# Kernel tuning notes

Hardware: AMD Instinct MI355X
Metric: run time of the kernel (lower is better)

## Reference

```python
import jax, jax.numpy as jnp
import numpy as np
import math

B = 262144
STATE = 6
TOTAL_MEAS = 27
HID = 256
INPUT_DIM = TOTAL_MEAS * 2 + 1 + STATE + 12  # 73
PI = math.pi
NORM_R_SCALE = 500.0 / 150000.0
ANG_IDX = np.array([0, 1, 3, 4, 6, 9, 10, 12, 13, 15, 18, 19, 21, 22, 24])
ANG_MASK = np.zeros((TOTAL_MEAS,), dtype=bool)
ANG_MASK[ANG_IDX] = True


def setup_inputs() -> dict:
    key = jax.random.key(0)
    ks = jax.random.split(key, 16)
    s = lambda fan: 1.0 / math.sqrt(fan)
    inp = {
        "meas": jax.random.normal(ks[0], (B, TOTAL_MEAS), jnp.float32),
        "mask": jnp.ones((B, TOTAL_MEAS), jnp.float32),
        "dt": jax.random.uniform(ks[1], (B,), jnp.float32),
        "baselines": jax.random.normal(ks[2], (B, 12), jnp.float32),
        "x_prev": jax.random.normal(ks[3], (B, STATE), jnp.float32),
        "hx": jnp.zeros((B, HID), jnp.float32),
        # GRU params (torch gate order: r, z, n)
        "W_ih": jax.random.uniform(ks[4], (3 * HID, INPUT_DIM), jnp.float32, -s(HID), s(HID)),
        "W_hh": jax.random.uniform(ks[5], (3 * HID, HID), jnp.float32, -s(HID), s(HID)),
        "b_ih": jax.random.uniform(ks[6], (3 * HID,), jnp.float32, -s(HID), s(HID)),
        "b_hh": jax.random.uniform(ks[7], (3 * HID,), jnp.float32, -s(HID), s(HID)),
        # LayerNorm
        "ln_g": jnp.ones((HID,), jnp.float32),
        "ln_b": jnp.zeros((HID,), jnp.float32),
        # MLP head: 256 -> 256 -> 128 -> 6*27
        "W1": jax.random.uniform(ks[8], (256, HID), jnp.float32, -s(HID), s(HID)),
        "b1": jax.random.uniform(ks[9], (256,), jnp.float32, -s(HID), s(HID)),
        "W2": jax.random.uniform(ks[10], (128, 256), jnp.float32, -s(256), s(256)),
        "b2": jax.random.uniform(ks[11], (128,), jnp.float32, -s(256), s(256)),
        "W3": jax.random.uniform(ks[12], (STATE * TOTAL_MEAS, 128), jnp.float32, -s(128), s(128)),
        "b3": jax.random.uniform(ks[13], (STATE * TOTAL_MEAS,), jnp.float32, -s(128), s(128)),
    }
    return inp


def _wrap_angle(a):
    two_pi = 2.0 * PI
    return a - two_pi * jnp.round(a / two_pi)


def _platform_y_pred(x_rel):
    # x_rel: [B, 6] -> [B, 9] radar/EO measurement
    r_xy = jnp.sqrt(x_rel[:, 0] ** 2 + x_rel[:, 2] ** 2 + 1e-9)
    az = jnp.arctan2(x_rel[:, 2], x_rel[:, 0]) / PI
    el = jnp.arctan2(x_rel[:, 4], r_xy) / PI
    r = jnp.sqrt(x_rel[:, 0] ** 2 + x_rel[:, 2] ** 2 + x_rel[:, 4] ** 2 + 1e-9)
    z = jnp.zeros_like(r)
    return jnp.stack([az, el, r, az, el, z, az, z, z], axis=1)


def _forward(meas, mask, dt, baselines, x_prev, hx,
             W_ih, W_hh, b_ih, b_hh, ln_g, ln_b, W1, b1, W2, b2, W3, b3):
    # f_predict (CV model): x0 += dt*x1, x2 += dt*x3, x4 += dt*x5
    dt_scaled = dt * NORM_R_SCALE  # [B]
    zcol = jnp.zeros_like(x_prev[:, :1])
    shift = jnp.concatenate([x_prev[:, 1:2], zcol, x_prev[:, 3:4], zcol, x_prev[:, 5:6], zcol], axis=1)
    x_minus = x_prev + dt_scaled[:, None] * shift  # [B, 6]

    y_pred = jnp.concatenate([
        _platform_y_pred(x_minus),
        _platform_y_pred(x_minus - baselines[:, 0:6]),
        _platform_y_pred(x_minus - baselines[:, 6:12]),
    ], axis=1)  # [B, 27]

    innov = meas - y_pred
    wrapped = _wrap_angle(innov * PI) / PI
    innov = jnp.where(jnp.asarray(ANG_MASK)[None, :], wrapped, innov)
    innov = innov * mask

    rnn_in = jnp.concatenate([innov, mask, dt[:, None], x_minus, baselines], axis=1)  # [B, 73]

    # single-step GRU (torch semantics, gate order r,z,n)
    gi = rnn_in @ W_ih.T + b_ih  # [B, 3H]
    gh = hx @ W_hh.T + b_hh      # [B, 3H]
    gi_r, gi_z, gi_n = jnp.split(gi, 3, axis=1)
    gh_r, gh_z, gh_n = jnp.split(gh, 3, axis=1)
    r = jax.nn.sigmoid(gi_r + gh_r)
    z = jax.nn.sigmoid(gi_z + gh_z)
    n = jnp.tanh(gi_n + r * gh_n)
    h_new = (1.0 - z) * n + z * hx  # [B, H]

    # LayerNorm
    mu = jnp.mean(h_new, axis=-1, keepdims=True)
    var = jnp.var(h_new, axis=-1, keepdims=True)
    h_ln = (h_new - mu) / jnp.sqrt(var + 1e-5) * ln_g + ln_b

    # MLP gain head (dropout inactive at inference)
    f1 = jax.nn.relu(h_ln @ W1.T + b1)
    f2 = jax.nn.relu(f1 @ W2.T + b2)
    K = (f2 @ W3.T + b3).reshape(-1, STATE, TOTAL_MEAS)
    K = jnp.clip(K, -3.0, 3.0)

    correction = jnp.einsum('bsm,bm->bs', K, innov)
    x_new = jnp.clip(x_minus + correction, -5.0, 5.0)
    return x_new, h_new


def reference(meas, mask, dt, baselines, x_prev, hx,
              W_ih, W_hh, b_ih, b_hh, ln_g, ln_b, W1, b1, W2, b2, W3, b3):
    return _forward(meas, mask, dt, baselines, x_prev, hx,
                    W_ih, W_hh, b_ih, b_hh, ln_g, ln_b, W1, b1, W2, b2, W3, b3)
```

## Files before the change

### kernel.cpp

```cpp
#include <hip/hip_runtime.h>
#include <math.h>

#define B_TOTAL  262144
#define ROWS     64
#define NWG      (B_TOTAL/ROWS)
#define NTHR     512
#define PI_F     3.14159265358979323846f
#define NORM_R   (500.0f/150000.0f)

typedef float  f32x4  __attribute__((ext_vector_type(4)));
typedef short  bf16x8 __attribute__((ext_vector_type(8)));

#define GRU_SLAB 24576
#define OFF_GRU  0
#define OFF_W1   (11*GRU_SLAB)
#define OFF_W2   (OFF_W1 + 8*8192)
#define OFF_W3   (OFF_W2 + 8*4096)
#define W_TOTAL  (OFF_W3 + 4*8192)

#define LDS_RBF2  0
#define LDS_HB    17408
#define LDS_STG   (LDS_HB + 32768)
#define LDS_XMC   (LDS_STG + 2*49152)
#define LDS_LNS   (LDS_XMC + 1536)
#define LDS_TOTAL (LDS_LNS + 2048)

#define WAIT_VM0 asm volatile("s_waitcnt vmcnt(0)" ::: "memory")
#define BARv     __builtin_amdgcn_s_barrier()

__device__ __forceinline__ ushort f2bf(float f){
    union { float f; unsigned u; } v; v.f = f;
    unsigned r = v.u + 0x7FFFu + ((v.u >> 16) & 1u);
    return (ushort)(r >> 16);
}
__device__ __forceinline__ float b2f(ushort u){
    union { unsigned u; float f; } v; v.u = ((unsigned)u) << 16;
    return v.f;
}
__device__ __forceinline__ float sigm(float x){ return 1.0f/(1.0f+__expf(-x)); }
__device__ __forceinline__ float tanh_(float x){ return 1.0f - 2.0f/(__expf(2.0f*x)+1.0f); }
__device__ __forceinline__ int swzb(int row, int k){
    return ((row<<9) + (k<<1)) ^ ((row&7)<<4);
}
__device__ __forceinline__ bf16x8 rdW(const char* gb, int col, int lk){
    int slot = lk ^ ((col >> 1) & 3);
    return *(const bf16x8*)(gb + col*64 + slot*16);
}
template<int N>
__device__ __forceinline__ void stage_lin(const ushort* src, char* dst, int w, int lane){
    #pragma unroll
    for (int i = 0; i < N; ++i) {
        __builtin_amdgcn_global_load_lds(
            (const __attribute__((address_space(1))) void*)(src + (size_t)(i*512 + w*64 + lane)*8),
            (__attribute__((address_space(3))) void*)(dst + i*8192 + w*1024),
            16, 0, 0);
    }
}
__device__ __forceinline__ void mm4(const char* gb, int colbase, int lr, int lk,
                                    bf16x8 a0, bf16x8 a1, f32x4 acc[2][4]){
    #pragma unroll
    for (int j = 0; j < 4; ++j) {
        bf16x8 wf = rdW(gb, colbase + j*16 + lr, lk);
        acc[0][j] = __builtin_amdgcn_mfma_f32_16x16x32_bf16(wf, a0, acc[0][j], 0,0,0);
        acc[1][j] = __builtin_amdgcn_mfma_f32_16x16x32_bf16(wf, a1, acc[1][j], 0,0,0);
    }
}

__global__ void prep_weights(const float* __restrict__ W_ih, const float* __restrict__ W_hh,
                             const float* __restrict__ W1, const float* __restrict__ W2,
                             const float* __restrict__ W3, ushort* __restrict__ ws)
{
    int id = blockIdx.x*256 + threadIdx.x;
    if (id >= W_TOTAL) return;
    float v = 0.0f;
    if (id < OFF_W1) {
        int slab = id / GRU_SLAB, u = id % GRU_SLAB;
        int gate = u >> 13, u2 = u & 8191;
        int col = u2 >> 5, v5 = u2 & 31, slot = v5 >> 3, e = v5 & 7;
        int kq = slot ^ ((col >> 1) & 3);
        int k = slab*32 + kq*8 + e;
        int rowz = gate*256 + col;
        v = (k < 73) ? W_ih[rowz*73 + k] : ((k < 96) ? 0.0f : W_hh[rowz*256 + (k-96)]);
    } else if (id < OFF_W2) {
        int t = id - OFF_W1, kb = t >> 13, u2 = t & 8191;
        int col = u2 >> 5, v5 = u2 & 31, slot = v5 >> 3, e = v5 & 7;
        int kq = slot ^ ((col >> 1) & 3);
        v = W1[col*256 + kb*32 + kq*8 + e];
    } else if (id < OFF_W3) {
        int t = id - OFF_W2, kb = t >> 12, u2 = t & 4095;
        int col = u2 >> 5, v5 = u2 & 31, slot = v5 >> 3, e = v5 & 7;
        int kq = slot ^ ((col >> 1) & 3);
        v = W2[col*256 + kb*32 + kq*8 + e];
    } else {
        int t = id - OFF_W3, kb = t >> 13, u2 = t & 8191;
        int col = u2 >> 5, v5 = u2 & 31, slot = v5 >> 3, e = v5 & 7;
        int kq = slot ^ ((col >> 1) & 3);
        int k = kb*32 + kq*8 + e;
        v = (col < 162) ? W3[col*128 + k] : 0.0f;
    }
    ws[id] = f2bf(v);
}

__global__ __launch_bounds__(NTHR, 1) void knet_mfma(
    const float* __restrict__ meas, const float* __restrict__ mask,
    const float* __restrict__ dt,   const float* __restrict__ baselines,
    const float* __restrict__ x_prev, const float* __restrict__ hx,
    const float* __restrict__ b_ih, const float* __restrict__ b_hh,
    const float* __restrict__ ln_g, const float* __restrict__ ln_b,
    const float* __restrict__ b1,   const float* __restrict__ b2,
    const float* __restrict__ b3,
    const ushort* __restrict__ ws,
    float* __restrict__ out)
{
    extern __shared__ char smem[];
    ushort* Rbu  = (ushort*)(smem + LDS_RBF2);
    char*   Hb   = smem + LDS_HB;
    char*   STG  = smem + LDS_STG;
    float*  xmc  = (float*)(smem + LDS_XMC);
    float*  lnscr= (float*)(smem + LDS_LNS);

    const int tid  = threadIdx.x;
    const int w    = __builtin_amdgcn_readfirstlane(tid >> 6);
    const int nq   = w & 3;
    const int mh   = w >> 2;
    const int lane = tid & 63;
    const int lr   = lane & 15;
    const int lk   = lane >> 4;
    const int lk8  = lk * 8;
    const int row0 = blockIdx.x * ROWS;
    const int mrow = mh*32 + lr;
    float* hout = out + (size_t)B_TOTAL*6;

    stage_lin<6>(ws + OFF_GRU, STG, w, lane);

    float* scr = (float*)(STG + 49152);
    {
        const size_t m0 = (size_t)row0*27;
        for (int i = tid; i < 1728; i += NTHR) scr[i]        = meas[m0 + i];
        for (int i = tid; i < 1728; i += NTHR) scr[1728 + i] = mask[m0 + i];
        const size_t b0 = (size_t)row0*12;
        for (int i = tid; i < 768; i += NTHR)  scr[3456 + i] = baselines[b0 + i];
        if (tid < 384) scr[4224 + tid] = x_prev[(size_t)row0*6 + tid];
        if (tid < 64)  scr[4608 + tid] = dt[row0 + tid];
        const size_t hbase = (size_t)row0 * 256;
        #pragma unroll
        for (int ii = 0; ii < 4; ++ii) {
            int cid = tid + ii*NTHR;
            int r  = cid >> 5;
            int k0 = (cid & 31) << 3;
            const float4* p = (const float4*)(hx + hbase + (size_t)r*256 + k0);
            float4 u = p[0], v2 = p[1];
            bf16x8 o;
            o[0]=(short)f2bf(u.x);  o[1]=(short)f2bf(u.y);  o[2]=(short)f2bf(u.z);  o[3]=(short)f2bf(u.w);
            o[4]=(short)f2bf(v2.x); o[5]=(short)f2bf(v2.y); o[6]=(short)f2bf(v2.z); o[7]=(short)f2bf(v2.w);
            *(bf16x8*)(Hb + swzb(r, k0)) = o;
        }
    }
    __syncthreads();

    if (w < 4) {
        const int row = lane;
        const float dtv = scr[4608 + row];
        const float dts = dtv * NORM_R;
        float xp[6], xm[6];
        #pragma unroll
        for (int s = 0; s < 6; ++s) xp[s] = scr[4224 + row*6 + s];
        xm[0] = xp[0] + dts*xp[1]; xm[1] = xp[1];
        xm[2] = xp[2] + dts*xp[3]; xm[3] = xp[3];
        xm[4] = xp[4] + dts*xp[5]; xm[5] = xp[5];
        if (w < 3) {
            float xr[6];
            #pragma unroll
            for (int s = 0; s < 6; ++s) {
                float b = (w == 0) ? 0.0f : scr[3456 + row*12 + (w-1)*6 + s];
                xr[s] = xm[s] - b;
            }
            float rxy = sqrtf(xr[0]*xr[0] + xr[2]*xr[2] + 1e-9f);
            float azv = atan2f(xr[2], xr[0]) * (1.0f/PI_F);
            float elv = atan2f(xr[4], rxy)   * (1.0f/PI_F);
            float rrv = sqrtf(xr[0]*xr[0] + xr[2]*xr[2] + xr[4]*xr[4] + 1e-9f);
            float y[9] = {azv, elv, rrv, azv, elv, 0.0f, azv, 0.0f, 0.0f};
            const bool ang[9] = {true,true,false,true,true,false,true,false,false};
            #pragma unroll
            for (int i = 0; i < 9; ++i) {
                int m = w*9 + i;
                float ms = scr[1728 + row*27 + m];
                float v  = scr[row*27 + m] - y[i];
                if (ang[i]) v = v - 2.0f*rintf(v*0.5f);
                v *= ms;
                Rbu[row*104 + m]      = f2bf(v);
                Rbu[row*104 + 27 + m] = f2bf(ms);
            }
        } else {
            Rbu[row*104 + 54] = f2bf(dtv);
            #pragma unroll
            for (int s = 0; s < 6; ++s) Rbu[row*104 + 55 + s] = f2bf(xm[s]);
            #pragma unroll
            for (int q = 0; q < 12; ++q) Rbu[row*104 + 61 + q] = f2bf(scr[3456 + row*12 + q]);
            #pragma unroll
            for (int k = 73; k < 96; ++k) Rbu[row*104 + k] = 0;
            #pragma unroll
            for (int s = 0; s < 6; ++s) xmc[row*6 + s] = xm[s];
        }
    }
    __syncthreads();

    f32x4 ar[2][4], az[2][4], agi[2][4], agh[2][4];
    #pragma unroll
    for (int i = 0; i < 2; ++i)
        #pragma unroll
        for (int j = 0; j < 4; ++j) {
            ar[i][j]=(f32x4){0,0,0,0}; az[i][j]=(f32x4){0,0,0,0};
            agi[i][j]=(f32x4){0,0,0,0}; agh[i][j]=(f32x4){0,0,0,0};
        }
    #pragma unroll
    for (int kb = 0; kb < 11; ++kb) {
        WAIT_VM0; BARv;
        if (kb < 10) stage_lin<6>(ws + OFF_GRU + (kb+1)*GRU_SLAB, STG + ((kb+1)&1)*49152, w, lane);
        else         stage_lin<6>(ws + OFF_W1,                    STG + 49152,            w, lane);
        const char* sb = STG + (kb&1)*49152;
        bf16x8 a0, a1;
        if (kb < 3) { a0 = *(const bf16x8*)(Rbu + mrow*104 + kb*32 + lk8);
                      a1 = *(const bf16x8*)(Rbu + (mrow+16)*104 + kb*32 + lk8); }
        else        { a0 = *(const bf16x8*)(Hb + swzb(mrow,    (kb-3)*32 + lk8));
                      a1 = *(const bf16x8*)(Hb + swzb(mrow+16, (kb-3)*32 + lk8)); }
        __builtin_amdgcn_s_setprio(1);
        mm4(sb,         nq*64, lr, lk, a0, a1, ar);
        mm4(sb + 16384, nq*64, lr, lk, a0, a1, az);
        if (kb < 3) mm4(sb + 32768, nq*64, lr, lk, a0, a1, agi);
        else        mm4(sb + 32768, nq*64, lr, lk, a0, a1, agh);
        __builtin_amdgcn_s_setprio(0);
    }

    f32x4 hnv[2][4];
    float lsum[2] = {0,0}, lsq[2] = {0,0};
    #pragma unroll
    for (int j = 0; j < 4; ++j) {
        const int c0 = nq*64 + j*16 + lk*4;
        f32x4 bir = *(const f32x4*)(b_ih + c0),        bhr = *(const f32x4*)(b_hh + c0);
        f32x4 biz = *(const f32x4*)(b_ih + 256 + c0),  bhz = *(const f32x4*)(b_hh + 256 + c0);
        f32x4 bin_= *(const f32x4*)(b_ih + 512 + c0),  bhn = *(const f32x4*)(b_hh + 512 + c0);
        #pragma unroll
        for (int i = 0; i < 2; ++i) {
            const int row = mh*32 + i*16 + lr;
            uint2 hxd = *(const uint2*)(Hb + swzb(row, c0));
            float hx_[4] = { b2f((ushort)(hxd.x & 0xffffu)), b2f((ushort)(hxd.x >> 16)),
                             b2f((ushort)(hxd.y & 0xffffu)), b2f((ushort)(hxd.y >> 16)) };
            f32x4 hn4;
            #pragma unroll
            for (int e = 0; e < 4; ++e) {
                float rg = sigm(ar[i][j][e] + bir[e] + bhr[e]);
                float zg = sigm(az[i][j][e] + biz[e] + bhz[e]);
                float ng = tanh_(agi[i][j][e] + bin_[e] + rg*(agh[i][j][e] + bhn[e]));
                float hn = (1.0f - zg)*ng + zg*hx_[e];
                hn4[e] = hn;
                lsum[i] += hn; lsq[i] += hn*hn;
            }
            hnv[i][j] = hn4;
            float4 st = { hn4[0], hn4[1], hn4[2], hn4[3] };
            *(float4*)(hout + (size_t)(row0+row)*256 + c0) = st;
        }
    }
    #pragma unroll
    for (int i = 0; i < 2; ++i) {
        lsum[i] += __shfl_xor(lsum[i], 16); lsum[i] += __shfl_xor(lsum[i], 32);
        lsq[i]  += __shfl_xor(lsq[i], 16);  lsq[i]  += __shfl_xor(lsq[i], 32);
    }
    if (lk == 0) {
        #pragma unroll
        for (int i = 0; i < 2; ++i) {
            const int row = mh*32 + i*16 + lr;
            lnscr[row*8 + nq*2 + 0] = lsum[i];
            lnscr[row*8 + nq*2 + 1] = lsq[i];
        }
    }
    __syncthreads();

    {
        float mu[2], rstd[2];
        #pragma unroll
        for (int i = 0; i < 2; ++i) {
            const int row = mh*32 + i*16 + lr;
            float s = 0, q = 0;
            #pragma unroll
            for (int qq = 0; qq < 4; ++qq) { s += lnscr[row*8 + qq*2]; q += lnscr[row*8 + qq*2 + 1]; }
            mu[i] = s * (1.0f/256.0f);
            rstd[i] = rsqrtf(q*(1.0f/256.0f) - mu[i]*mu[i] + 1e-5f);
        }
        #pragma unroll
        for (int j = 0; j < 4; ++j) {
            const int c0 = nq*64 + j*16 + lk*4;
            f32x4 g4 = *(const f32x4*)(ln_g + c0);
            f32x4 b4 = *(const f32x4*)(ln_b + c0);
            #pragma unroll
            for (int i = 0; i < 2; ++i) {
                const int row = mh*32 + i*16 + lr;
                float v0 = (hnv[i][j][0]-mu[i])*rstd[i]*g4[0] + b4[0];
                float v1 = (hnv[i][j][1]-mu[i])*rstd[i]*g4[1] + b4[1];
                float v2 = (hnv[i][j][2]-mu[i])*rstd[i]*g4[2] + b4[2];
                float v3 = (hnv[i][j][3]-mu[i])*rstd[i]*g4[3] + b4[3];
                uint2 o;
                o.x = (unsigned)f2bf(v0) | ((unsigned)f2bf(v1) << 16);
                o.y = (unsigned)f2bf(v2) | ((unsigned)f2bf(v3) << 16);
                *(uint2*)(Hb + swzb(row, c0)) = o;
            }
        }
    }
    __syncthreads();

    f32x4 c2[2][4];
    #pragma unroll
    for (int i = 0; i < 2; ++i)
        #pragma unroll
        for (int j = 0; j < 4; ++j) c2[i][j] = (f32x4){0,0,0,0};
    WAIT_VM0; BARv;
    stage_lin<6>(ws + OFF_W1 + 3*8192, STG, w, lane);
    {
        const char* sb = STG + 49152;
        #pragma unroll
        for (int kb = 0; kb < 3; ++kb) {
            bf16x8 a0 = *(const bf16x8*)(Hb + swzb(mrow,    kb*32 + lk8));
            bf16x8 a1 = *(const bf16x8*)(Hb + swzb(mrow+16, kb*32 + lk8));
            __builtin_amdgcn_s_setprio(1);
            mm4(sb + kb*16384, nq*64, lr, lk, a0, a1, c2);
            __builtin_amdgcn_s_setprio(0);
        }
    }
    WAIT_VM0; BARv;
    stage_lin<4>(ws + OFF_W1 + 6*8192, STG + 49152, w, lane);
    {
        const char* sb = STG;
        #pragma unroll
        for (int kb = 3; kb < 6; ++kb) {
            bf16x8 a0 = *(const bf16x8*)(Hb + swzb(mrow,    kb*32 + lk8));
            bf16x8 a1 = *(const bf16x8*)(Hb + swzb(mrow+16, kb*32 + lk8));
            __builtin_amdgcn_s_setprio(1);
            mm4(sb + (kb-3)*16384, nq*64, lr, lk, a0, a1, c2);
            __builtin_amdgcn_s_setprio(0);
        }
    }
    WAIT_VM0; BARv;
    stage_lin<4>(ws + OFF_W2, STG, w, lane);
    {
        const char* sb = STG + 49152;
        #pragma unroll
        for (int kb = 6; kb < 8; ++kb) {
            bf16x8 a0 = *(const bf16x8*)(Hb + swzb(mrow,    kb*32 + lk8));
            bf16x8 a1 = *(const bf16x8*)(Hb + swzb(mrow+16, kb*32 + lk8));
            __builtin_amdgcn_s_setprio(1);
            mm4(sb + (kb-6)*16384, nq*64, lr, lk, a0, a1, c2);
            __builtin_amdgcn_s_setprio(0);
        }
    }
    __syncthreads();
    #pragma unroll
    for (int j = 0; j < 4; ++j) {
        const int c0 = nq*64 + j*16 + lk*4;
        f32x4 b4 = *(const f32x4*)(b1 + c0);
        #pragma unroll
        for (int i = 0; i < 2; ++i) {
            const int row = mh*32 + i*16 + lr;
            uint2 o;
            o.x = (unsigned)f2bf(fmaxf(c2[i][j][0]+b4[0],0.f)) | ((unsigned)f2bf(fmaxf(c2[i][j][1]+b4[1],0.f)) << 16);
            o.y = (unsigned)f2bf(fmaxf(c2[i][j][2]+b4[2],0.f)) | ((unsigned)f2bf(fmaxf(c2[i][j][3]+b4[3],0.f)) << 16);
            *(uint2*)(Hb + swzb(row, c0)) = o;
        }
    }
    __syncthreads();

    f32x4 c3[2][2];
    #pragma unroll
    for (int i = 0; i < 2; ++i)
        #pragma unroll
        for (int j = 0; j < 2; ++j) c3[i][j] = (f32x4){0,0,0,0};
    WAIT_VM0; BARv;
    stage_lin<4>(ws + OFF_W2 + 4*4096, STG + 49152, w, lane);
    {
        const char* sb = STG;
        #pragma unroll
        for (int kb = 0; kb < 4; ++kb) {
            bf16x8 a0 = *(const bf16x8*)(Hb + swzb(mrow,    kb*32 + lk8));
            bf16x8 a1 = *(const bf16x8*)(Hb + swzb(mrow+16, kb*32 + lk8));
            __builtin_amdgcn_s_setprio(1);
            #pragma unroll
            for (int j = 0; j < 2; ++j) {
                bf16x8 wf = rdW(sb + kb*8192, nq*32 + j*16 + lr, lk);
                c3[0][j] = __builtin_amdgcn_mfma_f32_16x16x32_bf16(wf, a0, c3[0][j], 0,0,0);
                c3[1][j] = __builtin_amdgcn_mfma_f32_16x16x32_bf16(wf, a1, c3[1][j], 0,0,0);
            }
            __builtin_amdgcn_s_setprio(0);
        }
    }
    WAIT_VM0; BARv;
    stage_lin<4>(ws + OFF_W3, STG, w, lane);
    {
        const char* sb = STG + 49152;
        #pragma unroll
        for (int kb = 4; kb < 8; ++kb) {
            bf16x8 a0 = *(const bf16x8*)(Hb + swzb(mrow,    kb*32 + lk8));
            bf16x8 a1 = *(const bf16x8*)(Hb + swzb(mrow+16, kb*32 + lk8));
            __builtin_amdgcn_s_setprio(1);
            #pragma unroll
            for (int j = 0; j < 2; ++j) {
                bf16x8 wf = rdW(sb + (kb-4)*8192, nq*32 + j*16 + lr, lk);
                c3[0][j] = __builtin_amdgcn_mfma_f32_16x16x32_bf16(wf, a0, c3[0][j], 0,0,0);
                c3[1][j] = __builtin_amdgcn_mfma_f32_16x16x32_bf16(wf, a1, c3[1][j], 0,0,0);
            }
            __builtin_amdgcn_s_setprio(0);
        }
    }
    f32x4 iv[2][3];
    #pragma unroll
    for (int j = 0; j < 3; ++j) {
        #pragma unroll
        for (int i = 0; i < 2; ++i) {
            const int row = mh*32 + i*16 + lr;
            #pragma unroll
            for (int e = 0; e < 4; ++e) {
                int col = nq*48 + j*16 + lk*4 + e;
                int m = col - 27*(col/27);
                iv[i][j][e] = b2f(Rbu[row*104 + m]);
            }
        }
    }
    __syncthreads();
    #pragma unroll
    for (int j = 0; j < 2; ++j) {
        const int c0 = nq*32 + j*16 + lk*4;
        f32x4 b4 = *(const f32x4*)(b2 + c0);
        #pragma unroll
        for (int i = 0; i < 2; ++i) {
            const int row = mh*32 + i*16 + lr;
            uint2 o;
            o.x = (unsigned)f2bf(fmaxf(c3[i][j][0]+b4[0],0.f)) | ((unsigned)f2bf(fmaxf(c3[i][j][1]+b4[1],0.f)) << 16);
            o.y = (unsigned)f2bf(fmaxf(c3[i][j][2]+b4[2],0.f)) | ((unsigned)f2bf(fmaxf(c3[i][j][3]+b4[3],0.f)) << 16);
            *(uint2*)((char*)Rbu + row*272 + c0*2) = o;
        }
    }
    __syncthreads();

    f32x4 c4[2][3];
    #pragma unroll
    for (int i = 0; i < 2; ++i)
        #pragma unroll
        for (int j = 0; j < 3; ++j) c4[i][j] = (f32x4){0,0,0,0};
    WAIT_VM0; BARv;
    stage_lin<4>(ws + OFF_W3 + 2*8192, STG + 49152, w, lane);
    {
        const char* sb = STG;
        #pragma unroll
        for (int kb = 0; kb < 2; ++kb) {
            bf16x8 a0 = *(const bf16x8*)((char*)Rbu + (mrow     )*272 + (kb*32 + lk8)*2);
            bf16x8 a1 = *(const bf16x8*)((char*)Rbu + (mrow + 16)*272 + (kb*32 + lk8)*2);
            __builtin_amdgcn_s_setprio(1);
            #pragma unroll
            for (int j = 0; j < 3; ++j) {
                bf16x8 wf = rdW(sb + kb*16384, nq*48 + j*16 + lr, lk);
                c4[0][j] = __builtin_amdgcn_mfma_f32_16x16x32_bf16(wf, a0, c4[0][j], 0,0,0);
                c4[1][j] = __builtin_amdgcn_mfma_f32_16x16x32_bf16(wf, a1, c4[1][j], 0,0,0);
            }
            __builtin_amdgcn_s_setprio(0);
        }
    }
    WAIT_VM0; BARv;
    {
        const char* sb = STG + 49152;
        #pragma unroll
        for (int kb = 2; kb < 4; ++kb) {
            bf16x8 a0 = *(const bf16x8*)((char*)Rbu + (mrow     )*272 + (kb*32 + lk8)*2);
            bf16x8 a1 = *(const bf16x8*)((char*)Rbu + (mrow + 16)*272 + (kb*32 + lk8)*2);
            __builtin_amdgcn_s_setprio(1);
            #pragma unroll
            for (int j = 0; j < 3; ++j) {
                bf16x8 wf = rdW(sb + (kb-2)*16384, nq*48 + j*16 + lr, lk);
                c4[0][j] = __builtin_amdgcn_mfma_f32_16x16x32_bf16(wf, a0, c4[0][j], 0,0,0);
                c4[1][j] = __builtin_amdgcn_mfma_f32_16x16x32_bf16(wf, a1, c4[1][j], 0,0,0);
            }
            __builtin_amdgcn_s_setprio(0);
        }
    }
    #pragma unroll
    for (int j = 0; j < 3; ++j) {
        #pragma unroll
        for (int i = 0; i < 2; ++i) {
            const int row = mh*32 + i*16 + lr;
            #pragma unroll
            for (int e = 0; e < 4; ++e) {
                int col = nq*48 + j*16 + lk*4 + e;
                if (col < 162) {
                    int s = col / 27;
                    float K = fminf(fmaxf(c4[i][j][e] + b3[col], -3.0f), 3.0f);
                    atomicAdd(&xmc[row*6 + s], K * iv[i][j][e]);
                }
            }
        }
    }
    __syncthreads();

    for (int t = tid; t < ROWS*6; t += NTHR) {
        int row = t / 6, s = t - row*6;
        float v = fminf(fmaxf(xmc[t], -5.0f), 5.0f);
        out[(size_t)(row0+row)*6 + s] = v;
    }
}

extern "C" void kernel_launch(void* const* d_in, const int* in_sizes, int n_in,
                              void* d_out, int out_size, void* d_ws, size_t ws_size,
                              hipStream_t stream) {
    const float* meas      = (const float*)d_in[0];
    const float* mask      = (const float*)d_in[1];
    const float* dtv       = (const float*)d_in[2];
    const float* baselines = (const float*)d_in[3];
    const float* x_prev    = (const float*)d_in[4];
    const float* hx        = (const float*)d_in[5];
    const float* W_ih      = (const float*)d_in[6];
    const float* W_hh      = (const float*)d_in[7];
    const float* b_ih      = (const float*)d_in[8];
    const float* b_hh      = (const float*)d_in[9];
    const float* ln_g      = (const float*)d_in[10];
    const float* ln_b      = (const float*)d_in[11];
    const float* W1        = (const float*)d_in[12];
    const float* b1        = (const float*)d_in[13];
    const float* W2        = (const float*)d_in[14];
    const float* b2        = (const float*)d_in[15];
    const float* W3        = (const float*)d_in[16];
    const float* b3        = (const float*)d_in[17];
    ushort* wsb = (ushort*)d_ws;
    float* outp = (float*)d_out;

    prep_weights<<<(W_TOTAL + 255)/256, 256, 0, stream>>>(W_ih, W_hh, W1, W2, W3, wsb);
    knet_mfma<<<NWG, NTHR, LDS_TOTAL, stream>>>(
        meas, mask, dtv, baselines, x_prev, hx,
        b_ih, b_hh, ln_g, ln_b, b1, b2, b3, wsb, outp);
}
```

Measured before the change: 693.0 us.

## Double rows per workgroup and stage weights through registers into one LDS buffer

Measured after the change: 1.291 ms. +86.2%, slower.

```diff
diff --git a/kernel.cpp b/kernel.cpp
--- a/kernel.cpp
+++ b/kernel.cpp
@@ -2,7 +2,7 @@
 #include <math.h>
 
 #define B_TOTAL  262144
-#define ROWS     64
+#define ROWS     128
 #define NWG      (B_TOTAL/ROWS)
 #define NTHR     512
 #define PI_F     3.14159265358979323846f
@@ -11,22 +11,22 @@
 typedef float  f32x4  __attribute__((ext_vector_type(4)));
 typedef short  bf16x8 __attribute__((ext_vector_type(8)));
 
-#define GRU_SLAB 24576
-#define OFF_GRU  0
-#define OFF_W1   (11*GRU_SLAB)
-#define OFF_W2   (OFF_W1 + 8*8192)
-#define OFF_W3   (OFF_W2 + 8*4096)
-#define W_TOTAL  (OFF_W3 + 4*8192)
-
-#define LDS_RBF2  0
-#define LDS_HB    17408
-#define LDS_STG   (LDS_HB + 32768)
-#define LDS_XMC   (LDS_STG + 2*49152)
-#define LDS_LNS   (LDS_XMC + 1536)
-#define LDS_TOTAL (LDS_LNS + 2048)
-
-#define WAIT_VM0 asm volatile("s_waitcnt vmcnt(0)" ::: "memory")
-#define BARv     __builtin_amdgcn_s_barrier()
+#define OFF_GA 0
+#define OFF_GB 73728
+#define OFF_NH 204800
+#define OFF_W1 270336
+#define OFF_W2 335872
+#define OFF_W3 368640
+#define W_TOTAL 401408
+
+#define LDS_RB   0
+#define LDS_HB   34816
+#define LDS_STG  100352
+#define LDS_XMC  149504
+#define LDS_LNS  152576
+#define LDS_TOTAL 156672
+
+#define BARv __builtin_amdgcn_s_barrier()
 
 __device__ __forceinline__ ushort f2bf(float f){
     union { float f; unsigned u; } v; v.f = f;
@@ -46,23 +46,38 @@
     int slot = lk ^ ((col >> 1) & 3);
     return *(const bf16x8*)(gb + col*64 + slot*16);
 }
+
 template<int N>
-__device__ __forceinline__ void stage_lin(const ushort* src, char* dst, int w, int lane){
-    #pragma unroll
-    for (int i = 0; i < N; ++i) {
-        __builtin_amdgcn_global_load_lds(
-            (const __attribute__((address_space(1))) void*)(src + (size_t)(i*512 + w*64 + lane)*8),
-            (__attribute__((address_space(3))) void*)(dst + i*8192 + w*1024),
-            16, 0, 0);
-    }
-}
-__device__ __forceinline__ void mm4(const char* gb, int colbase, int lr, int lk,
-                                    bf16x8 a0, bf16x8 a1, f32x4 acc[2][4]){
+__device__ __forceinline__ void stg_issue(const ushort* src, uint4* rg, int w, int lane){
+    #pragma unroll
+    for (int i = 0; i < N; ++i)
+        rg[i] = *(const uint4*)(src + (size_t)(i*512 + w*64 + lane)*8);
+}
+template<int N>
+__device__ __forceinline__ void stg_commit(char* STG, const uint4* rg, int w, int lane){
+    #pragma unroll
+    for (int i = 0; i < N; ++i)
+        *(uint4*)(STG + i*8192 + w*1024 + lane*16) = rg[i];
+}
+
+__device__ __forceinline__ void ldA_rb(const ushort* Rbu, int mh, int lr, int kb, int lk8, bf16x8 a[4]){
+    #pragma unroll
+    for (int i = 0; i < 4; ++i)
+        a[i] = *(const bf16x8*)(Rbu + (mh*64 + i*16 + lr)*104 + kb*32 + lk8);
+}
+__device__ __forceinline__ void ldA_hb(const char* Hb, int mh, int lr, int kb, int lk8, bf16x8 a[4]){
+    #pragma unroll
+    for (int i = 0; i < 4; ++i)
+        a[i] = *(const bf16x8*)(Hb + swzb(mh*64 + i*16 + lr, kb*32 + lk8));
+}
+__device__ __forceinline__ void mmW(const char* base, int colbase, int lr, int lk,
+                                    const bf16x8 a[4], f32x4 acc[4][4]){
     #pragma unroll
     for (int j = 0; j < 4; ++j) {
-        bf16x8 wf = rdW(gb, colbase + j*16 + lr, lk);
-        acc[0][j] = __builtin_amdgcn_mfma_f32_16x16x32_bf16(wf, a0, acc[0][j], 0,0,0);
-        acc[1][j] = __builtin_amdgcn_mfma_f32_16x16x32_bf16(wf, a1, acc[1][j], 0,0,0);
+        bf16x8 wf = rdW(base, colbase + j*16 + lr, lk);
+        #pragma unroll
+        for (int i = 0; i < 4; ++i)
+            acc[i][j] = __builtin_amdgcn_mfma_f32_16x16x32_bf16(wf, a[i], acc[i][j], 0,0,0);
     }
 }
 
@@ -73,30 +88,51 @@
     int id = blockIdx.x*256 + threadIdx.x;
     if (id >= W_TOTAL) return;
     float v = 0.0f;
-    if (id < OFF_W1) {
-        int slab = id / GRU_SLAB, u = id % GRU_SLAB;
-        int gate = u >> 13, u2 = u & 8191;
+    if (id < OFF_GB) {
+        int slab = id / 24576, u = id % 24576;
+        int g = u >> 13, u2 = u & 8191;
         int col = u2 >> 5, v5 = u2 & 31, slot = v5 >> 3, e = v5 & 7;
         int kq = slot ^ ((col >> 1) & 3);
         int k = slab*32 + kq*8 + e;
-        int rowz = gate*256 + col;
-        v = (k < 73) ? W_ih[rowz*73 + k] : ((k < 96) ? 0.0f : W_hh[rowz*256 + (k-96)]);
+        if (g < 2) {
+            int rowz = g*256 + col;
+            v = (k < 73) ? W_ih[rowz*73 + k] : 0.0f;
+        } else {
+            v = (k < 73) ? W_ih[(512+col)*73 + k] : 0.0f;
+        }
+    } else if (id < OFF_NH) {
+        int t = id - OFF_GB;
+        int slab = t >> 14, u = t & 16383;
+        int kb = slab + 3;
+        int g = u >> 13, u2 = u & 8191;
+        int col = u2 >> 5, v5 = u2 & 31, slot = v5 >> 3, e = v5 & 7;
+        int kq = slot ^ ((col >> 1) & 3);
+        int k = kb*32 + kq*8 + e;
+        v = W_hh[(g*256 + col)*256 + (k - 96)];
+    } else if (id < OFF_W1) {
+        int t = id - OFF_NH;
+        int s = t >> 13, u2 = t & 8191;
+        int col = u2 >> 5, v5 = u2 & 31, slot = v5 >> 3, e = v5 & 7;
+        int kq = slot ^ ((col >> 1) & 3);
+        v = W_hh[(512 + col)*256 + s*32 + kq*8 + e];
     } else if (id < OFF_W2) {
-        int t = id - OFF_W1, kb = t >> 13, u2 = t & 8191;
+        int t = id - OFF_W1;
+        int kb = t >> 13, u2 = t & 8191;
         int col = u2 >> 5, v5 = u2 & 31, slot = v5 >> 3, e = v5 & 7;
         int kq = slot ^ ((col >> 1) & 3);
         v = W1[col*256 + kb*32 + kq*8 + e];
     } else if (id < OFF_W3) {
-        int t = id - OFF_W2, kb = t >> 12, u2 = t & 4095;
+        int t = id - OFF_W2;
+        int kb = t >> 12, u2 = t & 4095;
         int col = u2 >> 5, v5 = u2 & 31, slot = v5 >> 3, e = v5 & 7;
         int kq = slot ^ ((col >> 1) & 3);
         v = W2[col*256 + kb*32 + kq*8 + e];
     } else {
-        int t = id - OFF_W3, kb = t >> 13, u2 = t & 8191;
+        int t = id - OFF_W3;
+        int kb = t >> 13, u2 = t & 8191;
         int col = u2 >> 5, v5 = u2 & 31, slot = v5 >> 3, e = v5 & 7;
         int kq = slot ^ ((col >> 1) & 3);
-        int k = kb*32 + kq*8 + e;
-        v = (col < 162) ? W3[col*128 + k] : 0.0f;
+        v = (col < 162) ? W3[col*128 + kb*32 + kq*8 + e] : 0.0f;
     }
     ws[id] = f2bf(v);
 }
@@ -113,7 +149,7 @@
     float* __restrict__ out)
 {
     extern __shared__ char smem[];
-    ushort* Rbu  = (ushort*)(smem + LDS_RBF2);
+    ushort* Rbu  = (ushort*)(smem + LDS_RB);
     char*   Hb   = smem + LDS_HB;
     char*   STG  = smem + LDS_STG;
     float*  xmc  = (float*)(smem + LDS_XMC);
@@ -128,23 +164,80 @@
     const int lk   = lane >> 4;
     const int lk8  = lk * 8;
     const int row0 = blockIdx.x * ROWS;
-    const int mrow = mh*32 + lr;
     float* hout = out + (size_t)B_TOTAL*6;
 
-    stage_lin<6>(ws + OFF_GRU, STG, w, lane);
-
-    float* scr = (float*)(STG + 49152);
+    uint4 rg[6];
+
+    #pragma unroll
+    for (int i = 0; i < 6; ++i)
+        __builtin_amdgcn_global_load_lds(
+            (const __attribute__((address_space(1))) void*)(ws + OFF_GA + (size_t)(i*512 + w*64 + lane)*8),
+            (__attribute__((address_space(3))) void*)(STG + i*8192 + w*1024),
+            16, 0, 0);
+
+    float* scr = (float*)Hb;
     {
         const size_t m0 = (size_t)row0*27;
-        for (int i = tid; i < 1728; i += NTHR) scr[i]        = meas[m0 + i];
-        for (int i = tid; i < 1728; i += NTHR) scr[1728 + i] = mask[m0 + i];
-        const size_t b0 = (size_t)row0*12;
-        for (int i = tid; i < 768; i += NTHR)  scr[3456 + i] = baselines[b0 + i];
-        if (tid < 384) scr[4224 + tid] = x_prev[(size_t)row0*6 + tid];
-        if (tid < 64)  scr[4608 + tid] = dt[row0 + tid];
+        for (int i = tid; i < 3456; i += NTHR) scr[i]        = meas[m0 + i];
+        for (int i = tid; i < 3456; i += NTHR) scr[3456 + i] = mask[m0 + i];
+        for (int i = tid; i < 1536; i += NTHR) scr[6912 + i] = baselines[(size_t)row0*12 + i];
+        for (int i = tid; i < 768;  i += NTHR) scr[8448 + i] = x_prev[(size_t)row0*6 + i];
+        if (tid < 128) scr[9216 + tid] = dt[row0 + tid];
+    }
+    __syncthreads();
+
+    {
+        const int part = w >> 1;
+        const int row  = (w & 1)*64 + lane;
+        const float dtv = scr[9216 + row];
+        const float dts = dtv * NORM_R;
+        float xp[6], xm[6];
+        #pragma unroll
+        for (int s = 0; s < 6; ++s) xp[s] = scr[8448 + row*6 + s];
+        xm[0] = xp[0] + dts*xp[1]; xm[1] = xp[1];
+        xm[2] = xp[2] + dts*xp[3]; xm[3] = xp[3];
+        xm[4] = xp[4] + dts*xp[5]; xm[5] = xp[5];
+        if (part < 3) {
+            float xr[6];
+            #pragma unroll
+            for (int s = 0; s < 6; ++s) {
+                float b = (part == 0) ? 0.0f : scr[6912 + row*12 + (part-1)*6 + s];
+                xr[s] = xm[s] - b;
+            }
+            float rxy = sqrtf(xr[0]*xr[0] + xr[2]*xr[2] + 1e-9f);
+            float azv = atan2f(xr[2], xr[0]) * (1.0f/PI_F);
+            float elv = atan2f(xr[4], rxy)   * (1.0f/PI_F);
+            float rrv = sqrtf(xr[0]*xr[0] + xr[2]*xr[2] + xr[4]*xr[4] + 1e-9f);
+            float y[9] = {azv, elv, rrv, azv, elv, 0.0f, azv, 0.0f, 0.0f};
+            const bool ang[9] = {true,true,false,true,true,false,true,false,false};
+            #pragma unroll
+            for (int i = 0; i < 9; ++i) {
+                int m = part*9 + i;
+                float ms = scr[3456 + row*27 + m];
+                float v  = scr[row*27 + m] - y[i];
+                if (ang[i]) v = v - 2.0f*rintf(v*0.5f);
+                v *= ms;
+                Rbu[row*104 + m]      = f2bf(v);
+                Rbu[row*104 + 27 + m] = f2bf(ms);
+            }
+        } else {
+            Rbu[row*104 + 54] = f2bf(dtv);
+            #pragma unroll
+            for (int s = 0; s < 6; ++s) Rbu[row*104 + 55 + s] = f2bf(xm[s]);
+            #pragma unroll
+            for (int q = 0; q < 12; ++q) Rbu[row*104 + 61 + q] = f2bf(scr[6912 + row*12 + q]);
+            #pragma unroll
+            for (int k = 73; k < 96; ++k) Rbu[row*104 + k] = 0;
+            #pragma unroll
+            for (int s = 0; s < 6; ++s) xmc[row*6 + s] = xm[s];
+        }
+    }
+    __syncthreads();
+
+    {
         const size_t hbase = (size_t)row0 * 256;
         #pragma unroll
-        for (int ii = 0; ii < 4; ++ii) {
+        for (int ii = 0; ii < 8; ++ii) {
             int cid = tid + ii*NTHR;
             int r  = cid >> 5;
             int k0 = (cid & 31) << 3;
@@ -158,103 +251,104 @@
     }
     __syncthreads();
 
-    if (w < 4) {
-        const int row = lane;
-        const float dtv = scr[4608 + row];
-        const float dts = dtv * NORM_R;
-        float xp[6], xm[6];
-        #pragma unroll
-        for (int s = 0; s < 6; ++s) xp[s] = scr[4224 + row*6 + s];
-        xm[0] = xp[0] + dts*xp[1]; xm[1] = xp[1];
-        xm[2] = xp[2] + dts*xp[3]; xm[3] = xp[3];
-        xm[4] = xp[4] + dts*xp[5]; xm[5] = xp[5];
-        if (w < 3) {
-            float xr[6];
-            #pragma unroll
-            for (int s = 0; s < 6; ++s) {
-                float b = (w == 0) ? 0.0f : scr[3456 + row*12 + (w-1)*6 + s];
-                xr[s] = xm[s] - b;
-            }
-            float rxy = sqrtf(xr[0]*xr[0] + xr[2]*xr[2] + 1e-9f);
-            float azv = atan2f(xr[2], xr[0]) * (1.0f/PI_F);
-            float elv = atan2f(xr[4], rxy)   * (1.0f/PI_F);
-            float rrv = sqrtf(xr[0]*xr[0] + xr[2]*xr[2] + xr[4]*xr[4] + 1e-9f);
-            float y[9] = {azv, elv, rrv, azv, elv, 0.0f, azv, 0.0f, 0.0f};
-            const bool ang[9] = {true,true,false,true,true,false,true,false,false};
-            #pragma unroll
-            for (int i = 0; i < 9; ++i) {
-                int m = w*9 + i;
-                float ms = scr[1728 + row*27 + m];
-                float v  = scr[row*27 + m] - y[i];
-                if (ang[i]) v = v - 2.0f*rintf(v*0.5f);
-                v *= ms;
-                Rbu[row*104 + m]      = f2bf(v);
-                Rbu[row*104 + 27 + m] = f2bf(ms);
-            }
-        } else {
-            Rbu[row*104 + 54] = f2bf(dtv);
-            #pragma unroll
-            for (int s = 0; s < 6; ++s) Rbu[row*104 + 55 + s] = f2bf(xm[s]);
-            #pragma unroll
-            for (int q = 0; q < 12; ++q) Rbu[row*104 + 61 + q] = f2bf(scr[3456 + row*12 + q]);
-            #pragma unroll
-            for (int k = 73; k < 96; ++k) Rbu[row*104 + k] = 0;
-            #pragma unroll
-            for (int s = 0; s < 6; ++s) xmc[row*6 + s] = xm[s];
-        }
-    }
-    __syncthreads();
-
-    f32x4 ar[2][4], az[2][4], agi[2][4], agh[2][4];
-    #pragma unroll
-    for (int i = 0; i < 2; ++i)
+    f32x4 ar[4][4], az[4][4], gi[4][4], gh[4][4];
+    #pragma unroll
+    for (int i = 0; i < 4; ++i)
         #pragma unroll
         for (int j = 0; j < 4; ++j) {
             ar[i][j]=(f32x4){0,0,0,0}; az[i][j]=(f32x4){0,0,0,0};
-            agi[i][j]=(f32x4){0,0,0,0}; agh[i][j]=(f32x4){0,0,0,0};
-        }
-    #pragma unroll
-    for (int kb = 0; kb < 11; ++kb) {
-        WAIT_VM0; BARv;
-        if (kb < 10) stage_lin<6>(ws + OFF_GRU + (kb+1)*GRU_SLAB, STG + ((kb+1)&1)*49152, w, lane);
-        else         stage_lin<6>(ws + OFF_W1,                    STG + 49152,            w, lane);
-        const char* sb = STG + (kb&1)*49152;
-        bf16x8 a0, a1;
-        if (kb < 3) { a0 = *(const bf16x8*)(Rbu + mrow*104 + kb*32 + lk8);
-                      a1 = *(const bf16x8*)(Rbu + (mrow+16)*104 + kb*32 + lk8); }
-        else        { a0 = *(const bf16x8*)(Hb + swzb(mrow,    (kb-3)*32 + lk8));
-                      a1 = *(const bf16x8*)(Hb + swzb(mrow+16, (kb-3)*32 + lk8)); }
+            gi[i][j]=(f32x4){0,0,0,0}; gh[i][j]=(f32x4){0,0,0,0};
+        }
+
+    #pragma unroll
+    for (int kb = 0; kb < 3; ++kb) {
+        if (kb < 2) stg_issue<6>(ws + OFF_GA + (kb+1)*24576, rg, w, lane);
+        else        stg_issue<4>(ws + OFF_GB,                rg, w, lane);
+        bf16x8 a[4];
+        ldA_rb(Rbu, mh, lr, kb, lk8, a);
         __builtin_amdgcn_s_setprio(1);
-        mm4(sb,         nq*64, lr, lk, a0, a1, ar);
-        mm4(sb + 16384, nq*64, lr, lk, a0, a1, az);
-        if (kb < 3) mm4(sb + 32768, nq*64, lr, lk, a0, a1, agi);
-        else        mm4(sb + 32768, nq*64, lr, lk, a0, a1, agh);
+        mmW(STG,         nq*64, lr, lk, a, ar);
+        mmW(STG + 16384, nq*64, lr, lk, a, az);
+        mmW(STG + 32768, nq*64, lr, lk, a, gi);
         __builtin_amdgcn_s_setprio(0);
-    }
-
-    f32x4 hnv[2][4];
-    float lsum[2] = {0,0}, lsq[2] = {0,0};
+        BARv;
+        if (kb < 2) stg_commit<6>(STG, rg, w, lane);
+        else        stg_commit<4>(STG, rg, w, lane);
+        __syncthreads();
+    }
+    #pragma unroll
+    for (int kb = 3; kb < 11; ++kb) {
+        if (kb < 10) stg_issue<4>(ws + OFF_GB + (kb-2)*16384, rg, w, lane);
+        else         stg_issue<4>(ws + OFF_NH,                rg, w, lane);
+        bf16x8 a[4];
+        ldA_hb(Hb, mh, lr, kb-3, lk8, a);
+        __builtin_amdgcn_s_setprio(1);
+        mmW(STG,         nq*64, lr, lk, a, ar);
+        mmW(STG + 16384, nq*64, lr, lk, a, az);
+        __builtin_amdgcn_s_setprio(0);
+        BARv;
+        stg_commit<4>(STG, rg, w, lane);
+        __syncthreads();
+    }
+
+    unsigned rzr[4][4][2], rzz[4][4][2];
     #pragma unroll
     for (int j = 0; j < 4; ++j) {
         const int c0 = nq*64 + j*16 + lk*4;
-        f32x4 bir = *(const f32x4*)(b_ih + c0),        bhr = *(const f32x4*)(b_hh + c0);
-        f32x4 biz = *(const f32x4*)(b_ih + 256 + c0),  bhz = *(const f32x4*)(b_hh + 256 + c0);
-        f32x4 bin_= *(const f32x4*)(b_ih + 512 + c0),  bhn = *(const f32x4*)(b_hh + 512 + c0);
-        #pragma unroll
-        for (int i = 0; i < 2; ++i) {
-            const int row = mh*32 + i*16 + lr;
+        f32x4 bi0 = *(const f32x4*)(b_ih + c0),       bh0 = *(const f32x4*)(b_hh + c0);
+        f32x4 bi1 = *(const f32x4*)(b_ih + 256 + c0), bh1 = *(const f32x4*)(b_hh + 256 + c0);
+        #pragma unroll
+        for (int i = 0; i < 4; ++i)
+            #pragma unroll
+            for (int eh = 0; eh < 2; ++eh) {
+                float r0 = sigm(ar[i][j][2*eh]   + bi0[2*eh]   + bh0[2*eh]);
+                float r1 = sigm(ar[i][j][2*eh+1] + bi0[2*eh+1] + bh0[2*eh+1]);
+                rzr[i][j][eh] = (unsigned)f2bf(r0) | ((unsigned)f2bf(r1) << 16);
+                float z0 = sigm(az[i][j][2*eh]   + bi1[2*eh]   + bh1[2*eh]);
+                float z1 = sigm(az[i][j][2*eh+1] + bi1[2*eh+1] + bh1[2*eh+1]);
+                rzz[i][j][eh] = (unsigned)f2bf(z0) | ((unsigned)f2bf(z1) << 16);
+            }
+    }
+
+    #pragma unroll
+    for (int p = 0; p < 4; ++p) {
+        if (p < 3) stg_issue<4>(ws + OFF_NH + (p+1)*16384, rg, w, lane);
+        else       stg_issue<4>(ws + OFF_W1,               rg, w, lane);
+        bf16x8 a[4];
+        ldA_hb(Hb, mh, lr, 2*p, lk8, a);
+        __builtin_amdgcn_s_setprio(1);
+        mmW(STG, nq*64, lr, lk, a, gh);
+        __builtin_amdgcn_s_setprio(0);
+        ldA_hb(Hb, mh, lr, 2*p+1, lk8, a);
+        __builtin_amdgcn_s_setprio(1);
+        mmW(STG + 16384, nq*64, lr, lk, a, gh);
+        __builtin_amdgcn_s_setprio(0);
+        BARv;
+        stg_commit<4>(STG, rg, w, lane);
+        __syncthreads();
+    }
+
+    f32x4 hnv[4][4];
+    float lsum[4] = {0,0,0,0}, lsq[4] = {0,0,0,0};
+    #pragma unroll
+    for (int j = 0; j < 4; ++j) {
+        const int c0 = nq*64 + j*16 + lk*4;
+        f32x4 bin4 = *(const f32x4*)(b_ih + 512 + c0);
+        f32x4 bhn4 = *(const f32x4*)(b_hh + 512 + c0);
+        #pragma unroll
+        for (int i = 0; i < 4; ++i) {
+            const int row = mh*64 + i*16 + lr;
             uint2 hxd = *(const uint2*)(Hb + swzb(row, c0));
             float hx_[4] = { b2f((ushort)(hxd.x & 0xffffu)), b2f((ushort)(hxd.x >> 16)),
                              b2f((ushort)(hxd.y & 0xffffu)), b2f((ushort)(hxd.y >> 16)) };
             f32x4 hn4;
             #pragma unroll
             for (int e = 0; e < 4; ++e) {
-                float rg = sigm(ar[i][j][e] + bir[e] + bhr[e]);
-                float zg = sigm(az[i][j][e] + biz[e] + bhz[e]);
-                float ng = tanh_(agi[i][j][e] + bin_[e] + rg*(agh[i][j][e] + bhn[e]));
-                float hn = (1.0f - zg)*ng + zg*hx_[e];
-                hn4[e] = hn;
-                lsum[i] += hn; lsq[i] += hn*hn;
+                float rgt = b2f((ushort)((rzr[i][j][e>>1] >> ((e&1)*16)) & 0xffffu));
+                float zgt = b2f((ushort)((rzz[i][j][e>>1] >> ((e&1)*16)) & 0xffffu));
+                float ng = tanh_(gi[i][j][e] + bin4[e] + rgt*(gh[i][j][e] + bhn4[e]));
+                float hn = (1.0f - zgt)*ng + zgt*hx_[e];
+                hn4[e] = hn; lsum[i] += hn; lsq[i] += hn*hn;
             }
             hnv[i][j] = hn4;
             float4 st = { hn4[0], hn4[1], hn4[2], hn4[3] };
@@ -262,14 +356,14 @@
         }
     }
     #pragma unroll
-    for (int i = 0; i < 2; ++i) {
+    for (int i = 0; i < 4; ++i) {
         lsum[i] += __shfl_xor(lsum[i], 16); lsum[i] += __shfl_xor(lsum[i], 32);
         lsq[i]  += __shfl_xor(lsq[i], 16);  lsq[i]  += __shfl_xor(lsq[i], 32);
     }
     if (lk == 0) {
         #pragma unroll
-        for (int i = 0; i < 2; ++i) {
-            const int row = mh*32 + i*16 + lr;
+        for (int i = 0; i < 4; ++i) {
+            const int row = mh*64 + i*16 + lr;
             lnscr[row*8 + nq*2 + 0] = lsum[i];
             lnscr[row*8 + nq*2 + 1] = lsq[i];
         }
@@ -277,10 +371,10 @@
     __syncthreads();
 
     {
-        float mu[2], rstd[2];
-        #pragma unroll
-        for (int i = 0; i < 2; ++i) {
-            const int row = mh*32 + i*16 + lr;
+        float mu[4], rstd[4];
+        #pragma unroll
+        for (int i = 0; i < 4; ++i) {
+            const int row = mh*64 + i*16 + lr;
             float s = 0, q = 0;
             #pragma unroll
             for (int qq = 0; qq < 4; ++qq) { s += lnscr[row*8 + qq*2]; q += lnscr[row*8 + qq*2 + 1]; }
@@ -293,8 +387,8 @@
             f32x4 g4 = *(const f32x4*)(ln_g + c0);
             f32x4 b4 = *(const f32x4*)(ln_b + c0);
             #pragma unroll
-            for (int i = 0; i < 2; ++i) {
-                const int row = mh*32 + i*16 + lr;
+            for (int i = 0; i < 4; ++i) {
+                const int row = mh*64 + i*16 + lr;
                 float v0 = (hnv[i][j][0]-mu[i])*rstd[i]*g4[0] + b4[0];
                 float v1 = (hnv[i][j][1]-mu[i])*rstd[i]*g4[1] + b4[1];
                 float v2 = (hnv[i][j][2]-mu[i])*rstd[i]*g4[2] + b4[2];
@@ -308,58 +402,35 @@
     }
     __syncthreads();
 
-    f32x4 c2[2][4];
-    #pragma unroll
-    for (int i = 0; i < 2; ++i)
+    f32x4 c2[4][4];
+    #pragma unroll
+    for (int i = 0; i < 4; ++i)
         #pragma unroll
         for (int j = 0; j < 4; ++j) c2[i][j] = (f32x4){0,0,0,0};
-    WAIT_VM0; BARv;
-    stage_lin<6>(ws + OFF_W1 + 3*8192, STG, w, lane);
-    {
-        const char* sb = STG + 49152;
-        #pragma unroll
-        for (int kb = 0; kb < 3; ++kb) {
-            bf16x8 a0 = *(const bf16x8*)(Hb + swzb(mrow,    kb*32 + lk8));
-            bf16x8 a1 = *(const bf16x8*)(Hb + swzb(mrow+16, kb*32 + lk8));
-            __builtin_amdgcn_s_setprio(1);
-            mm4(sb + kb*16384, nq*64, lr, lk, a0, a1, c2);
-            __builtin_amdgcn_s_setprio(0);
-        }
-    }
-    WAIT_VM0; BARv;
-    stage_lin<4>(ws + OFF_W1 + 6*8192, STG + 49152, w, lane);
-    {
-        const char* sb = STG;
-        #pragma unroll
-        for (int kb = 3; kb < 6; ++kb) {
-            bf16x8 a0 = *(const bf16x8*)(Hb + swzb(mrow,    kb*32 + lk8));
-            bf16x8 a1 = *(const bf16x8*)(Hb + swzb(mrow+16, kb*32 + lk8));
-            __builtin_amdgcn_s_setprio(1);
-            mm4(sb + (kb-3)*16384, nq*64, lr, lk, a0, a1, c2);
-            __builtin_amdgcn_s_setprio(0);
-        }
-    }
-    WAIT_VM0; BARv;
-    stage_lin<4>(ws + OFF_W2, STG, w, lane);
-    {
-        const char* sb = STG + 49152;
-        #pragma unroll
-        for (int kb = 6; kb < 8; ++kb) {
-            bf16x8 a0 = *(const bf16x8*)(Hb + swzb(mrow,    kb*32 + lk8));
-            bf16x8 a1 = *(const bf16x8*)(Hb + swzb(mrow+16, kb*32 + lk8));
-            __builtin_amdgcn_s_setprio(1);
-            mm4(sb + (kb-6)*16384, nq*64, lr, lk, a0, a1, c2);
-            __builtin_amdgcn_s_setprio(0);
-        }
-    }
-    __syncthreads();
+    #pragma unroll
+    for (int p = 0; p < 4; ++p) {
+        if (p < 3) stg_issue<4>(ws + OFF_W1 + (p+1)*16384, rg, w, lane);
+        else       stg_issue<4>(ws + OFF_W2,               rg, w, lane);
+        bf16x8 a[4];
+        ldA_hb(Hb, mh, lr, 2*p, lk8, a);
+        __builtin_amdgcn_s_setprio(1);
+        mmW(STG, nq*64, lr, lk, a, c2);
+        __builtin_amdgcn_s_setprio(0);
+        ldA_hb(Hb, mh, lr, 2*p+1, lk8, a);
+        __builtin_amdgcn_s_setprio(1);
+        mmW(STG + 16384, nq*64, lr, lk, a, c2);
+        __builtin_amdgcn_s_setprio(0);
+        BARv;
+        stg_commit<4>(STG, rg, w, lane);
+        __syncthreads();
+    }
     #pragma unroll
     for (int j = 0; j < 4; ++j) {
         const int c0 = nq*64 + j*16 + lk*4;
         f32x4 b4 = *(const f32x4*)(b1 + c0);
         #pragma unroll
-        for (int i = 0; i < 2; ++i) {
-            const int row = mh*32 + i*16 + lr;
+        for (int i = 0; i < 4; ++i) {
+            const int row = mh*64 + i*16 + lr;
             uint2 o;
             o.x = (unsigned)f2bf(fmaxf(c2[i][j][0]+b4[0],0.f)) | ((unsigned)f2bf(fmaxf(c2[i][j][1]+b4[1],0.f)) << 16);
             o.y = (unsigned)f2bf(fmaxf(c2[i][j][2]+b4[2],0.f)) | ((unsigned)f2bf(fmaxf(c2[i][j][3]+b4[3],0.f)) << 16);
@@ -368,53 +439,39 @@
     }
     __syncthreads();
 
-    f32x4 c3[2][2];
-    #pragma unroll
-    for (int i = 0; i < 2; ++i)
+    f32x4 c3[4][2];
+    #pragma unroll
+    for (int i = 0; i < 4; ++i)
         #pragma unroll
         for (int j = 0; j < 2; ++j) c3[i][j] = (f32x4){0,0,0,0};
-    WAIT_VM0; BARv;
-    stage_lin<4>(ws + OFF_W2 + 4*4096, STG + 49152, w, lane);
-    {
-        const char* sb = STG;
-        #pragma unroll
-        for (int kb = 0; kb < 4; ++kb) {
-            bf16x8 a0 = *(const bf16x8*)(Hb + swzb(mrow,    kb*32 + lk8));
-            bf16x8 a1 = *(const bf16x8*)(Hb + swzb(mrow+16, kb*32 + lk8));
+    #pragma unroll
+    for (int p = 0; p < 2; ++p) {
+        if (p == 0) stg_issue<4>(ws + OFF_W2 + 16384, rg, w, lane);
+        else        stg_issue<4>(ws + OFF_W3,         rg, w, lane);
+        #pragma unroll
+        for (int q = 0; q < 4; ++q) {
+            bf16x8 a[4];
+            ldA_hb(Hb, mh, lr, 4*p+q, lk8, a);
             __builtin_amdgcn_s_setprio(1);
             #pragma unroll
             for (int j = 0; j < 2; ++j) {
-                bf16x8 wf = rdW(sb + kb*8192, nq*32 + j*16 + lr, lk);
-                c3[0][j] = __builtin_amdgcn_mfma_f32_16x16x32_bf16(wf, a0, c3[0][j], 0,0,0);
-                c3[1][j] = __builtin_amdgcn_mfma_f32_16x16x32_bf16(wf, a1, c3[1][j], 0,0,0);
+                bf16x8 wf = rdW(STG + q*8192, nq*32 + j*16 + lr, lk);
+                #pragma unroll
+                for (int i = 0; i < 4; ++i)
+                    c3[i][j] = __builtin_amdgcn_mfma_f32_16x16x32_bf16(wf, a[i], c3[i][j], 0,0,0);
             }
             __builtin_amdgcn_s_setprio(0);
         }
-    }
-    WAIT_VM0; BARv;
-    stage_lin<4>(ws + OFF_W3, STG, w, lane);
-    {
-        const char* sb = STG + 49152;
-        #pragma unroll
-        for (int kb = 4; kb < 8; ++kb) {
-            bf16x8 a0 = *(const bf16x8*)(Hb + swzb(mrow,    kb*32 + lk8));
-            bf16x8 a1 = *(const bf16x8*)(Hb + swzb(mrow+16, kb*32 + lk8));
-            __builtin_amdgcn_s_setprio(1);
-            #pragma unroll
-            for (int j = 0; j < 2; ++j) {
-                bf16x8 wf = rdW(sb + (kb-4)*8192, nq*32 + j*16 + lr, lk);
-                c3[0][j] = __builtin_amdgcn_mfma_f32_16x16x32_bf16(wf, a0, c3[0][j], 0,0,0);
-                c3[1][j] = __builtin_amdgcn_mfma_f32_16x16x32_bf16(wf, a1, c3[1][j], 0,0,0);
-            }
-            __builtin_amdgcn_s_setprio(0);
-        }
-    }
-    f32x4 iv[2][3];
-    #pragma unroll
-    for (int j = 0; j < 3; ++j) {
-        #pragma unroll
-        for (int i = 0; i < 2; ++i) {
-            const int row = mh*32 + i*16 + lr;
+        BARv;
+        stg_commit<4>(STG, rg, w, lane);
+        __syncthreads();
+    }
+    f32x4 iv[4][3];
+    #pragma unroll
+    for (int j = 0; j < 3; ++j)
+        #pragma unroll
+        for (int i = 0; i < 4; ++i) {
+            const int row = mh*64 + i*16 + lr;
             #pragma unroll
             for (int e = 0; e < 4; ++e) {
                 int col = nq*48 + j*16 + lk*4 + e;
@@ -422,15 +479,14 @@
                 iv[i][j][e] = b2f(Rbu[row*104 + m]);
             }
         }
-    }
     __syncthreads();
     #pragma unroll
     for (int j = 0; j < 2; ++j) {
         const int c0 = nq*32 + j*16 + lk*4;
         f32x4 b4 = *(const f32x4*)(b2 + c0);
         #pragma unroll
-        for (int i = 0; i < 2; ++i) {
-            const int row = mh*32 + i*16 + lr;
+        for (int i = 0; i < 4; ++i) {
+            const int row = mh*64 + i*16 + lr;
             uint2 o;
             o.x = (unsigned)f2bf(fmaxf(c3[i][j][0]+b4[0],0.f)) | ((unsigned)f2bf(fmaxf(c3[i][j][1]+b4[1],0.f)) << 16);
             o.y = (unsigned)f2bf(fmaxf(c3[i][j][2]+b4[2],0.f)) | ((unsigned)f2bf(fmaxf(c3[i][j][3]+b4[3],0.f)) << 16);
@@ -439,51 +495,42 @@
     }
     __syncthreads();
 
-    f32x4 c4[2][3];
-    #pragma unroll
-    for (int i = 0; i < 2; ++i)
+    f32x4 c4[4][3];
+    #pragma unroll
+    for (int i = 0; i < 4; ++i)
         #pragma unroll
         for (int j = 0; j < 3; ++j) c4[i][j] = (f32x4){0,0,0,0};
-    WAIT_VM0; BARv;
-    stage_lin<4>(ws + OFF_W3 + 2*8192, STG + 49152, w, lane);
-    {
-        const char* sb = STG;
-        #pragma unroll
-        for (int kb = 0; kb < 2; ++kb) {
-            bf16x8 a0 = *(const bf16x8*)((char*)Rbu + (mrow     )*272 + (kb*32 + lk8)*2);
-            bf16x8 a1 = *(const bf16x8*)((char*)Rbu + (mrow + 16)*272 + (kb*32 + lk8)*2);
+    #pragma unroll
+    for (int p = 0; p < 2; ++p) {
+        if (p == 0) stg_issue<4>(ws + OFF_W3 + 16384, rg, w, lane);
+        #pragma unroll
+        for (int q = 0; q < 2; ++q) {
+            const int kb = 2*p + q;
+            bf16x8 a[4];
+            #pragma unroll
+            for (int i = 0; i < 4; ++i)
+                a[i] = *(const bf16x8*)((const char*)Rbu + (mh*64 + i*16 + lr)*272 + (kb*32 + lk8)*2);
             __builtin_amdgcn_s_setprio(1);
             #pragma unroll
             for (int j = 0; j < 3; ++j) {
-                bf16x8 wf = rdW(sb + kb*16384, nq*48 + j*16 + lr, lk);
-                c4[0][j] = __builtin_amdgcn_mfma_f32_16x16x32_bf16(wf, a0, c4[0][j], 0,0,0);
-                c4[1][j] = __builtin_amdgcn_mfma_f32_16x16x32_bf16(wf, a1, c4[1][j], 0,0,0);
+                bf16x8 wf = rdW(STG + q*16384, nq*48 + j*16 + lr, lk);
+                #pragma unroll
+                for (int i = 0; i < 4; ++i)
+                    c4[i][j] = __builtin_amdgcn_mfma_f32_16x16x32_bf16(wf, a[i], c4[i][j], 0,0,0);
             }
             __builtin_amdgcn_s_setprio(0);
         }
-    }
-    WAIT_VM0; BARv;
-    {
-        const char* sb = STG + 49152;
-        #pragma unroll
-        for (int kb = 2; kb < 4; ++kb) {
-            bf16x8 a0 = *(const bf16x8*)((char*)Rbu + (mrow     )*272 + (kb*32 + lk8)*2);
-            bf16x8 a1 = *(const bf16x8*)((char*)Rbu + (mrow + 16)*272 + (kb*32 + lk8)*2);
-            __builtin_amdgcn_s_setprio(1);
-            #pragma unroll
-            for (int j = 0; j < 3; ++j) {
-                bf16x8 wf = rdW(sb + (kb-2)*16384, nq*48 + j*16 + lr, lk);
-                c4[0][j] = __builtin_amdgcn_mfma_f32_16x16x32_bf16(wf, a0, c4[0][j], 0,0,0);
-                c4[1][j] = __builtin_amdgcn_mfma_f32_16x16x32_bf16(wf, a1, c4[1][j], 0,0,0);
-            }
-            __builtin_amdgcn_s_setprio(0);
-        }
-    }
-    #pragma unroll
-    for (int j = 0; j < 3; ++j) {
-        #pragma unroll
-        for (int i = 0; i < 2; ++i) {
-            const int row = mh*32 + i*16 + lr;
+        if (p == 0) {
+            BARv;
+            stg_commit<4>(STG, rg, w, lane);
+            __syncthreads();
+        }
+    }
+    #pragma unroll
+    for (int j = 0; j < 3; ++j)
+        #pragma unroll
+        for (int i = 0; i < 4; ++i) {
+            const int row = mh*64 + i*16 + lr;
             #pragma unroll
             for (int e = 0; e < 4; ++e) {
                 int col = nq*48 + j*16 + lk*4 + e;
@@ -494,7 +541,6 @@
                 }
             }
         }
-    }
     __syncthreads();
 
     for (int t = tid; t < ROWS*6; t += NTHR) {
```
